# Performance work log

Hardware: AMD Instinct MI355X
Metric: run time of the kernel (lower is better)

The kernel has to match this reference:

```python
import jax, jax.numpy as jnp
import numpy as np

N_NODES = 50000
N_EDGES = 800000
N_GRAPHS = 128
HEADS = 4
HDIM = 32
N_CLASSES = 10
LEAKY_ALPHA = 0.2


def setup_inputs() -> dict:
    key = jax.random.key(0)
    ks = jax.random.split(key, 12)
    src = jax.random.randint(ks[0], (N_EDGES,), 0, N_NODES, dtype=jnp.int32)
    # guarantee every node has in-degree >= 1 so 3/deg is finite
    dst_tail = jax.random.randint(ks[1], (N_EDGES - N_NODES,), 0, N_NODES, dtype=jnp.int32)
    dst = jnp.concatenate([jnp.arange(N_NODES, dtype=jnp.int32), dst_tail])
    graph_ids = jnp.sort(jax.random.randint(ks[2], (N_NODES,), 0, N_GRAPHS, dtype=jnp.int32))
    s = 0.1
    return {
        "src": src,
        "dst": dst,
        "graph_ids": graph_ids,
        "W1": jax.random.normal(ks[3], (4, HEADS * HDIM), jnp.float32) * s,
        "al1": jax.random.normal(ks[4], (HEADS, HDIM), jnp.float32) * s,
        "ar1": jax.random.normal(ks[5], (HEADS, HDIM), jnp.float32) * s,
        "W2": jax.random.normal(ks[6], (HEADS * HDIM, HEADS * HDIM), jnp.float32) * s,
        "al2": jax.random.normal(ks[7], (HEADS, HDIM), jnp.float32) * s,
        "ar2": jax.random.normal(ks[8], (HEADS, HDIM), jnp.float32) * s,
        "Wc": jax.random.normal(ks[9], (HEADS * HDIM, N_CLASSES), jnp.float32) * s,
        "bc": jax.random.normal(ks[10], (N_CLASSES,), jnp.float32) * s,
    }


def _gat_layer(x, src, dst, W, al, ar):
    # x: [N, Fin]; W: [Fin, H*D]; al, ar: [H, D]
    n = x.shape[0]
    ft = (x @ W).reshape(n, HEADS, HDIM)                       # [N, H, D]
    a1 = jnp.einsum("nhd,hd->nh", ft, al)                      # [N, H]
    a2 = jnp.einsum("nhd,hd->nh", ft, ar)                      # [N, H]
    e = jax.nn.leaky_relu(a1[src] + a2[dst], LEAKY_ALPHA)      # [E, H]
    # segment softmax over incoming edges of each dst node
    m = jax.ops.segment_max(e, dst, num_segments=n)            # [N, H]
    m = jax.lax.stop_gradient(m)
    ex = jnp.exp(e - m[dst])                                   # [E, H]
    denom = jax.ops.segment_sum(ex, dst, num_segments=n)       # [N, H]
    alpha = ex / denom[dst]                                    # [E, H]
    # gather-multiply-scatter aggregation
    out = jax.ops.segment_sum(ft[src] * alpha[:, :, None], dst, num_segments=n)  # [N, H, D]
    return jax.nn.relu(out.reshape(n, HEADS * HDIM))


def reference(src, dst, graph_ids, W1, al1, ar1, W2, al2, ar2, Wc, bc):
    n = N_NODES
    ones_e = jnp.ones(src.shape[0], jnp.float32)
    deg = jax.ops.segment_sum(ones_e, dst, num_segments=n)     # in-degrees [N]
    h = jnp.stack(
        [deg, (deg - 3.0 > 0).astype(jnp.float32), 3.0 / deg, (deg - 4.0 > 0).astype(jnp.float32)],
        axis=1,
    )                                                          # [N, 4]
    h = _gat_layer(h, src, dst, W1, al1, ar1)                  # [N, H*D]
    h = _gat_layer(h, src, dst, W2, al2, ar2)                  # [N, H*D]
    # mean_nodes: per-graph mean pooling
    gsum = jax.ops.segment_sum(h, graph_ids, num_segments=N_GRAPHS)
    cnt = jax.ops.segment_sum(jnp.ones(n, jnp.float32), graph_ids, num_segments=N_GRAPHS)
    gmean = gsum / jnp.maximum(cnt, 1.0)[:, None]              # [G, H*D]
    return jax.nn.sigmoid(gmean @ Wc + bc)                     # [G, n_classes]
```

## Files before the change

### kernel.cpp

```cpp
#include <hip/hip_runtime.h>
#include <hip/hip_fp16.h>
#include <math.h>

#define HEADS 4
#define HDIM 32
#define FDIM 128
#define NGRAPH 128
#define NCLASS 10

#define NBW 128
#define NBP 512
#define BCAP 4096
#define SLICE 4096

typedef _Float16 h4_t __attribute__((ext_vector_type(4)));
typedef float f4_t __attribute__((ext_vector_type(4)));
typedef float f2_t __attribute__((ext_vector_type(2)));

__device__ __forceinline__ float lrelu(float x) { return fmaxf(x, 0.2f * x); }

__global__ void k_wfrag(const float* __restrict__ W2, __half* __restrict__ Wfrag,
                        float* __restrict__ gsum, int* __restrict__ gcnt,
                        int* __restrict__ bcur) {
    int gid = blockIdx.x * 256 + threadIdx.x;
    ((float4*)gsum)[gid] = make_float4(0.f, 0.f, 0.f, 0.f);
    if (gid < NGRAPH) gcnt[gid] = 0;
    if (gid < NBP) bcur[gid] = 0;
    int fid = gid >> 6, l = gid & 63;
    int ks = fid >> 3, t = fid & 7;
    int k0 = ks * 16 + 4 * (l >> 4);
    int n0 = t * 16 + (l & 15);
    __half2 lo = __floats2half2_rn(W2[(k0 + 0) * FDIM + n0], W2[(k0 + 1) * FDIM + n0]);
    __half2 hi = __floats2half2_rn(W2[(k0 + 2) * FDIM + n0], W2[(k0 + 3) * FDIM + n0]);
    size_t base = ((size_t)fid * 64 + l) * 4;
    *(__half2*)(Wfrag + base)     = lo;
    *(__half2*)(Wfrag + base + 2) = hi;
}

__global__ __launch_bounds__(256) void k_part(const int* __restrict__ src,
        const int* __restrict__ dst, int E, int* __restrict__ bcur,
        unsigned int* __restrict__ part) {
    __shared__ int lcnt[NBP];
    __shared__ int loff[NBP];
    __shared__ int lpos[NBP];
    __shared__ unsigned int staged[SLICE];
    __shared__ int tgt[SLICE];
    __shared__ int ws[4];
    int tid = threadIdx.x, lane = tid & 63, w = tid >> 6;
    int beg = blockIdx.x * SLICE, end = min(E, beg + SLICE);
    int m = end - beg;
    for (int i = tid; i < NBP; i += 256) lcnt[i] = 0;
    __syncthreads();
    for (int i = beg + tid; i < end; i += 256)
        atomicAdd(&lcnt[dst[i] >> 7], 1);
    __syncthreads();
    int c0 = lcnt[2 * tid], c1 = lcnt[2 * tid + 1];
    int t = c0 + c1;
    int incl = t;
    #pragma unroll
    for (int off = 1; off < 64; off <<= 1) {
        int y = __shfl_up(incl, off);
        if (lane >= off) incl += y;
    }
    if (lane == 63) ws[w] = incl;
    __syncthreads();
    int wpre = 0;
    #pragma unroll
    for (int j = 0; j < 4; ++j) if (j < w) wpre += ws[j];
    int ex = wpre + (incl - t);
    loff[2 * tid] = ex; loff[2 * tid + 1] = ex + c0;
    if (c0) lpos[2 * tid] = atomicAdd(&bcur[2 * tid], c0);
    if (c1) lpos[2 * tid + 1] = atomicAdd(&bcur[2 * tid + 1], c1);
    lcnt[2 * tid] = 0; lcnt[2 * tid + 1] = 0;
    __syncthreads();
    for (int i = beg + tid; i < end; i += 256) {
        int s = src[i], d = dst[i];
        int b = d >> 7;
        int idx = atomicAdd(&lcnt[b], 1);
        int slot = loff[b] + idx;
        staged[slot] = ((unsigned int)(d & (NBW - 1)) << 16) | (unsigned int)s;
        tgt[slot] = b * BCAP + lpos[b] + idx;
    }
    __syncthreads();
    for (int i = tid; i < m; i += 256)
        part[tgt[i]] = staged[i];
}

__global__ __launch_bounds__(256) void k_build(const unsigned int* __restrict__ part,
        const int* __restrict__ bcur, unsigned int* __restrict__ nodeinfo,
        unsigned short* __restrict__ csr, unsigned short* __restrict__ deg16, int n) {
    __shared__ int ldeg[NBW];
    __shared__ int loffs[NBW];
    __shared__ int wtot[2];
    int b = blockIdx.x, tid = threadIdx.x;
    int lane = tid & 63, w = tid >> 6;
    if (tid < NBW) ldeg[tid] = 0;
    __syncthreads();
    int beg = b * BCAP, end = beg + bcur[b];
    for (int i = beg + tid; i < end; i += 256)
        atomicAdd(&ldeg[part[i] >> 16], 1);
    __syncthreads();
    int x = (tid < NBW) ? ldeg[tid] : 0;
    int incl = x;
    #pragma unroll
    for (int off = 1; off < 64; off <<= 1) {
        int y = __shfl_up(incl, off);
        if (lane >= off) incl += y;
    }
    if (tid < NBW && lane == 63) wtot[w] = incl;
    __syncthreads();
    if (tid < NBW) {
        int pre = incl - x;
        if (w == 1) pre += wtot[0];
        loffs[tid] = beg + pre;
        int v = b * NBW + tid;
        if (v < n) {
            nodeinfo[v] = ((unsigned int)(beg + pre) << 9) | (unsigned int)x;
            deg16[v] = (unsigned short)x;
        }
    }
    __syncthreads();
    if (tid < NBW) ldeg[tid] = 0;
    __syncthreads();
    for (int i = beg + tid; i < end; i += 256) {
        unsigned int e = part[i];
        int lv = e >> 16;
        int p = atomicAdd(&ldeg[lv], 1);
        csr[loffs[lv] + p] = (unsigned short)(e & 0xffffu);
    }
}

__global__ __launch_bounds__(256) void k_agg1(const unsigned int* __restrict__ nodeinfo,
        const unsigned short* __restrict__ csr, const unsigned short* __restrict__ deg16,
        const float* __restrict__ W1, const float* __restrict__ al1,
        const float* __restrict__ ar1, float* __restrict__ Sbuf, int n) {
    __shared__ float wla[16], wlr[16];
    int tid = threadIdx.x;
    if (tid < 32) {
        int k = (tid & 15) >> 2, h = tid & 3;
        const float* av = (tid < 16) ? al1 : ar1;
        float s = 0.f;
        #pragma unroll
        for (int d = 0; d < 32; ++d) s += W1[k * FDIM + h * HDIM + d] * av[h * HDIM + d];
        if (tid < 16) wla[k * 4 + h] = s; else wlr[k * 4 + h] = s;
    }
    __syncthreads();
    int c = tid & 15;
    int v = blockIdx.x * 16 + (tid >> 4);
    if (v >= n) return;
    unsigned int info = nodeinfo[v];
    int beg = info >> 9;
    int dg = info & 511;
    float dv = (float)dg;
    float4 hvv = make_float4(dv, (dv - 3.0f > 0.0f) ? 1.0f : 0.0f, 3.0f / dv,
                             (dv - 4.0f > 0.0f) ? 1.0f : 0.0f);
    float a2h[4];
    #pragma unroll
    for (int h = 0; h < 4; ++h)
        a2h[h] = hvv.x * wlr[0 + h] + hvv.y * wlr[4 + h] + hvv.z * wlr[8 + h] + hvv.w * wlr[12 + h];
    float P[4][4], D[4];
    #pragma unroll
    for (int h = 0; h < 4; ++h) { D[h] = 0.f;
        #pragma unroll
        for (int d = 0; d < 4; ++d) P[h][d] = 0.f; }
    for (int j = beg + c; j < beg + dg; j += 16) {
        int u = csr[j];
        float du = (float)deg16[u];
        float4 fu = make_float4(du, (du - 3.0f > 0.0f) ? 1.0f : 0.0f, 3.0f / du,
                                (du - 4.0f > 0.0f) ? 1.0f : 0.0f);
        float wgt[4];
        #pragma unroll
        for (int h = 0; h < 4; ++h) {
            float a1h = fu.x * wla[0 + h] + fu.y * wla[4 + h] + fu.z * wla[8 + h] + fu.w * wla[12 + h];
            wgt[h] = __expf(lrelu(a1h + a2h[h]));
        }
        #pragma unroll
        for (int h = 0; h < 4; ++h) {
            D[h] += wgt[h];
            P[h][0] = fmaf(wgt[h], fu.x, P[h][0]);
            P[h][1] = fmaf(wgt[h], fu.y, P[h][1]);
            P[h][2] = fmaf(wgt[h], fu.z, P[h][2]);
            P[h][3] = fmaf(wgt[h], fu.w, P[h][3]);
        }
    }
    #pragma unroll
    for (int off = 1; off < 16; off <<= 1) {
        #pragma unroll
        for (int h = 0; h < 4; ++h) {
            D[h] += __shfl_xor(D[h], off);
            #pragma unroll
            for (int d = 0; d < 4; ++d) P[h][d] += __shfl_xor(P[h][d], off);
        }
    }
    if (c == 0) {
        #pragma unroll
        for (int h = 0; h < 4; ++h) {
            float r = 1.0f / D[h];
            *(float4*)(Sbuf + v * 16 + h * 4) =
                make_float4(P[h][0] * r, P[h][1] * r, P[h][2] * r, P[h][3] * r);
        }
    }
}

__global__ __launch_bounds__(256) void k_layer2(const float* __restrict__ Sbuf,
        const float* __restrict__ W1, const __half* __restrict__ Wfrag,
        const float* __restrict__ al, const float* __restrict__ ar,
        unsigned char* __restrict__ ft8, float* __restrict__ a1b,
        float* __restrict__ a2b, int n) {
    __shared__ __half Alds[4][16 * 132];
    int tid = threadIdx.x, l = tid & 63, w = tid >> 6;
    int c = l & 15, g = l >> 4;
    int v0 = (blockIdx.x * 4 + w) * 16;

    float2 w1c[4];
    #pragma unroll
    for (int d = 0; d < 4; ++d) w1c[d] = *(const float2*)(W1 + d * FDIM + 2 * l);
    for (int jj = 0; jj < 16; ++jj) {
        int v = min(v0 + jj, n - 1);
        float4 s = *(const float4*)(Sbuf + (size_t)v * 16 + g * 4);
        float t0 = s.x * w1c[0].x + s.y * w1c[1].x + s.z * w1c[2].x + s.w * w1c[3].x;
        float t1 = s.x * w1c[0].y + s.y * w1c[1].y + s.z * w1c[2].y + s.w * w1c[3].y;
        *(__half2*)(&Alds[w][jj * 132 + 2 * l]) = __floats2half2_rn(fmaxf(t0, 0.f), fmaxf(t1, 0.f));
    }
    __syncthreads();

    f4_t acc[8];
    #pragma unroll
    for (int t = 0; t < 8; ++t) acc[t] = (f4_t){0.f, 0.f, 0.f, 0.f};
    #pragma unroll
    for (int ks = 0; ks < 8; ++ks) {
        h4_t af = *(const h4_t*)(&Alds[w][c * 132 + ks * 16 + 4 * g]);
        #pragma unroll
        for (int t = 0; t < 8; ++t) {
            h4_t bf = *(const h4_t*)(Wfrag + ((size_t)(ks * 8 + t) * 64 + l) * 4);
            acc[t] = __builtin_amdgcn_mfma_f32_16x16x16f16(af, bf, acc[t], 0, 0, 0);
        }
    }

    #pragma unroll
    for (int t = 0; t < 8; ++t) {
        #pragma unroll
        for (int r = 0; r < 4; ++r) {
            int v = v0 + 4 * g + r;
            if (v < n) {
                int pk = __builtin_amdgcn_cvt_pk_fp8_f32(acc[t][r], acc[t][r], 0, false);
                ft8[(size_t)v * FDIM + t * 16 + c] = (unsigned char)(pk & 0xff);
            }
        }
    }
    float al0[4], al1v[4], ar0[4], ar1v[4];
    #pragma unroll
    for (int h = 0; h < 4; ++h) {
        al0[h] = al[h * 32 + c]; al1v[h] = al[h * 32 + 16 + c];
        ar0[h] = ar[h * 32 + c]; ar1v[h] = ar[h * 32 + 16 + c];
    }
    #pragma unroll
    for (int r = 0; r < 4; ++r) {
        int v = v0 + 4 * g + r;
        #pragma unroll
        for (int h = 0; h < 4; ++h) {
            float p1 = acc[2 * h][r] * al0[h] + acc[2 * h + 1][r] * al1v[h];
            float p2 = acc[2 * h][r] * ar0[h] + acc[2 * h + 1][r] * ar1v[h];
            #pragma unroll
            for (int off = 1; off < 16; off <<= 1) {
                p1 += __shfl_xor(p1, off);
                p2 += __shfl_xor(p2, off);
            }
            if (c == h && v < n) {
                a1b[v * 4 + h] = p1;
                a2b[v * 4 + h] = p2;
            }
        }
    }
}

__global__ __launch_bounds__(256) void k_agg2(const unsigned int* __restrict__ nodeinfo,
        const unsigned short* __restrict__ csr, const unsigned char* __restrict__ ft8,
        const float* __restrict__ a1, const float* __restrict__ a2,
        __half* __restrict__ out, int n) {
    int tid = threadIdx.x, lane = tid & 63, w = tid >> 6;
    int qw = lane >> 4, ql = lane & 15;
    int v = blockIdx.x * 16 + w * 4 + qw;
    if (v >= n) return;
    unsigned int info = nodeinfo[v];
    int beg = info >> 9, end = beg + (info & 511);
    int h = ql >> 2;
    float a2h = a2[v * 4 + h];
    float acc[8];
    #pragma unroll
    for (int k = 0; k < 8; ++k) acc[k] = 0.f;
    float dsum = 0.f;
    const unsigned char* fbase = ft8 + (size_t)ql * 8;
    int j = beg;
    for (; j + 4 <= end; j += 4) {
        int s[4];
        #pragma unroll
        for (int k = 0; k < 4; ++k) s[k] = csr[j + k];
        float wv[4]; uint2 bv[4];
        #pragma unroll
        for (int k = 0; k < 4; ++k) {
            wv[k] = __expf(lrelu(a1[s[k] * 4 + h] + a2h));
            bv[k] = *(const uint2*)(fbase + (size_t)s[k] * FDIM);
        }
        #pragma unroll
        for (int k = 0; k < 4; ++k) {
            dsum += wv[k];
            f2_t g;
            g = __builtin_amdgcn_cvt_pk_f32_fp8(bv[k].x, false); acc[0] = fmaf(wv[k], g[0], acc[0]); acc[1] = fmaf(wv[k], g[1], acc[1]);
            g = __builtin_amdgcn_cvt_pk_f32_fp8(bv[k].x, true);  acc[2] = fmaf(wv[k], g[0], acc[2]); acc[3] = fmaf(wv[k], g[1], acc[3]);
            g = __builtin_amdgcn_cvt_pk_f32_fp8(bv[k].y, false); acc[4] = fmaf(wv[k], g[0], acc[4]); acc[5] = fmaf(wv[k], g[1], acc[5]);
            g = __builtin_amdgcn_cvt_pk_f32_fp8(bv[k].y, true);  acc[6] = fmaf(wv[k], g[0], acc[6]); acc[7] = fmaf(wv[k], g[1], acc[7]);
        }
    }
    for (; j < end; ++j) {
        int s0 = csr[j];
        float w0 = __expf(lrelu(a1[s0 * 4 + h] + a2h));
        uint2 b0 = *(const uint2*)(fbase + (size_t)s0 * FDIM);
        dsum += w0;
        f2_t g;
        g = __builtin_amdgcn_cvt_pk_f32_fp8(b0.x, false); acc[0] = fmaf(w0, g[0], acc[0]); acc[1] = fmaf(w0, g[1], acc[1]);
        g = __builtin_amdgcn_cvt_pk_f32_fp8(b0.x, true);  acc[2] = fmaf(w0, g[0], acc[2]); acc[3] = fmaf(w0, g[1], acc[3]);
        g = __builtin_amdgcn_cvt_pk_f32_fp8(b0.y, false); acc[4] = fmaf(w0, g[0], acc[4]); acc[5] = fmaf(w0, g[1], acc[5]);
        g = __builtin_amdgcn_cvt_pk_f32_fp8(b0.y, true);  acc[6] = fmaf(w0, g[0], acc[6]); acc[7] = fmaf(w0, g[1], acc[7]);
    }
    float r = 1.0f / dsum;
    __half2 o[4];
    #pragma unroll
    for (int k = 0; k < 4; ++k)
        o[k] = __floats2half2_rn(fmaxf(acc[2 * k] * r, 0.f), fmaxf(acc[2 * k + 1] * r, 0.f));
    *(float4*)(out + (size_t)v * FDIM + ql * 8) = *(float4*)o;
}

__global__ void k_pool(const __half* __restrict__ hbuf, const int* __restrict__ gid,
                       float* __restrict__ gsum, int* __restrict__ gcnt, int n) {
    const int STRIP = 32;
    int wv = (blockIdx.x * blockDim.x + threadIdx.x) >> 6;
    int lane = threadIdx.x & 63;
    int beg = wv * STRIP;
    if (beg >= n) return;
    int end = min(beg + STRIP, n);
    int f = 2 * lane;
    float2 acc = make_float2(0.f, 0.f);
    int cur = gid[beg];
    int cnt = 0;
    for (int i = beg; i < end; ++i) {
        int g = gid[i];
        if (g != cur) {
            atomicAdd(&gsum[cur * FDIM + f], acc.x);
            atomicAdd(&gsum[cur * FDIM + f + 1], acc.y);
            if (lane == 0) atomicAdd(&gcnt[cur], cnt);
            acc = make_float2(0.f, 0.f); cnt = 0; cur = g;
        }
        float2 x = __half22float2(*(const __half2*)(hbuf + (size_t)i * FDIM + f));
        acc.x += x.x; acc.y += x.y; cnt++;
    }
    atomicAdd(&gsum[cur * FDIM + f], acc.x);
    atomicAdd(&gsum[cur * FDIM + f + 1], acc.y);
    if (lane == 0) atomicAdd(&gcnt[cur], cnt);
}

__global__ void k_classify(const float* __restrict__ gsum, const int* __restrict__ gcnt,
                           const float* __restrict__ Wc, const float* __restrict__ bc,
                           float* __restrict__ out) {
    int idx = blockIdx.x * blockDim.x + threadIdx.x;
    if (idx >= NGRAPH * NCLASS) return;
    int g = idx / NCLASS, c = idx % NCLASS;
    float rc = 1.0f / fmaxf((float)gcnt[g], 1.0f);
    float s = bc[c];
    for (int k = 0; k < FDIM; ++k)
        s += gsum[g * FDIM + k] * rc * Wc[k * NCLASS + c];
    out[idx] = 1.0f / (1.0f + __expf(-s));
}

extern "C" void kernel_launch(void* const* d_in, const int* in_sizes, int n_in,
                              void* d_out, int out_size, void* d_ws, size_t ws_size,
                              hipStream_t stream) {
    const int*   src = (const int*)d_in[0];
    const int*   dst = (const int*)d_in[1];
    const int*   gid = (const int*)d_in[2];
    const float* W1  = (const float*)d_in[3];
    const float* al1 = (const float*)d_in[4];
    const float* ar1 = (const float*)d_in[5];
    const float* W2  = (const float*)d_in[6];
    const float* al2 = (const float*)d_in[7];
    const float* ar2 = (const float*)d_in[8];
    const float* Wc  = (const float*)d_in[9];
    const float* bc  = (const float*)d_in[10];
    float* out = (float*)d_out;
    const int E = in_sizes[0];
    const int N = in_sizes[2];

    char* ws = (char*)d_ws;
    size_t off = 0;
    auto alloc = [&](size_t bytes) -> void* {
        void* p = ws + off;
        off = (off + bytes + 255) & ~(size_t)255;
        return p;
    };
    unsigned int*   part = (unsigned int*)alloc((size_t)NBP * BCAP * 4);
    unsigned short* csr  = (unsigned short*)alloc((size_t)NBP * BCAP * 2);
    int*    bcur   = (int*)alloc(NBP * 4);
    unsigned int* nodeinfo = (unsigned int*)alloc((size_t)N * 4);
    unsigned short* deg16  = (unsigned short*)alloc((size_t)N * 2);
    float*  Sbuf   = (float*)alloc((size_t)N * 16 * 4);
    float*  a1b    = (float*)alloc((size_t)N * HEADS * 4);
    float*  a2b    = (float*)alloc((size_t)N * HEADS * 4);
    unsigned char* ft8 = (unsigned char*)alloc((size_t)N * FDIM);
    __half* hbuf   = (__half*)alloc((size_t)N * FDIM * 2);
    __half* Wfrag  = (__half*)alloc((size_t)FDIM * FDIM * 2);
    float*  gsum   = (float*)alloc((size_t)NGRAPH * FDIM * 4);
    int*    gcnt   = (int*)alloc((size_t)NGRAPH * 4);

    int pb_edges = (E + SLICE - 1) / SLICE;
    int nb2 = (N + NBW - 1) / NBW;

    k_wfrag<<<16, 256, 0, stream>>>(W2, Wfrag, gsum, gcnt, bcur);
    k_part<<<pb_edges, 256, 0, stream>>>(src, dst, E, bcur, part);
    k_build<<<nb2, 256, 0, stream>>>(part, bcur, nodeinfo, csr, deg16, N);
    k_agg1<<<(N + 15) / 16, 256, 0, stream>>>(nodeinfo, csr, deg16, W1, al1, ar1, Sbuf, N);
    k_layer2<<<(N + 63) / 64, 256, 0, stream>>>(Sbuf, W1, Wfrag, al2, ar2, ft8, a1b, a2b, N);
    k_agg2<<<(N + 15) / 16, 256, 0, stream>>>(nodeinfo, csr, ft8, a1b, a2b, hbuf, N);

    int pb = (((N + 31) / 32) + 3) / 4;
    k_pool<<<pb, 256, 0, stream>>>(hbuf, gid, gsum, gcnt, N);
    k_classify<<<(NGRAPH * NCLASS + 255) / 256, 256, 0, stream>>>(gsum, gcnt, Wc, bc, out);
}
```

Before: 119.5 us.

## Split layer-2 GEMM output columns across wave pairs to double block count

```diff
diff --git a/kernel.cpp b/kernel.cpp
--- a/kernel.cpp
+++ b/kernel.cpp
@@ -207,68 +207,69 @@
         const float* __restrict__ al, const float* __restrict__ ar,
         unsigned char* __restrict__ ft8, float* __restrict__ a1b,
         float* __restrict__ a2b, int n) {
-    __shared__ __half Alds[4][16 * 132];
+    __shared__ __half Alds[2][16 * 132];
     int tid = threadIdx.x, l = tid & 63, w = tid >> 6;
+    int g2 = w >> 1, half = w & 1;
     int c = l & 15, g = l >> 4;
-    int v0 = (blockIdx.x * 4 + w) * 16;
+    int v0 = (blockIdx.x * 2 + g2) * 16;
 
     float2 w1c[4];
     #pragma unroll
     for (int d = 0; d < 4; ++d) w1c[d] = *(const float2*)(W1 + d * FDIM + 2 * l);
-    for (int jj = 0; jj < 16; ++jj) {
+    #pragma unroll
+    for (int jr = 0; jr < 8; ++jr) {
+        int jj = half * 8 + jr;
         int v = min(v0 + jj, n - 1);
         float4 s = *(const float4*)(Sbuf + (size_t)v * 16 + g * 4);
         float t0 = s.x * w1c[0].x + s.y * w1c[1].x + s.z * w1c[2].x + s.w * w1c[3].x;
         float t1 = s.x * w1c[0].y + s.y * w1c[1].y + s.z * w1c[2].y + s.w * w1c[3].y;
-        *(__half2*)(&Alds[w][jj * 132 + 2 * l]) = __floats2half2_rn(fmaxf(t0, 0.f), fmaxf(t1, 0.f));
-    }
-    __syncthreads();
-
-    f4_t acc[8];
-    #pragma unroll
-    for (int t = 0; t < 8; ++t) acc[t] = (f4_t){0.f, 0.f, 0.f, 0.f};
+        *(__half2*)(&Alds[g2][jj * 132 + 2 * l]) = __floats2half2_rn(fmaxf(t0, 0.f), fmaxf(t1, 0.f));
+    }
+    __syncthreads();
+
+    f4_t acc[4];
+    #pragma unroll
+    for (int t = 0; t < 4; ++t) acc[t] = (f4_t){0.f, 0.f, 0.f, 0.f};
     #pragma unroll
     for (int ks = 0; ks < 8; ++ks) {
-        h4_t af = *(const h4_t*)(&Alds[w][c * 132 + ks * 16 + 4 * g]);
-        #pragma unroll
-        for (int t = 0; t < 8; ++t) {
-            h4_t bf = *(const h4_t*)(Wfrag + ((size_t)(ks * 8 + t) * 64 + l) * 4);
+        h4_t af = *(const h4_t*)(&Alds[g2][c * 132 + ks * 16 + 4 * g]);
+        #pragma unroll
+        for (int t = 0; t < 4; ++t) {
+            h4_t bf = *(const h4_t*)(Wfrag + ((size_t)(ks * 8 + half * 4 + t) * 64 + l) * 4);
             acc[t] = __builtin_amdgcn_mfma_f32_16x16x16f16(af, bf, acc[t], 0, 0, 0);
         }
     }
 
     #pragma unroll
-    for (int t = 0; t < 8; ++t) {
+    for (int t = 0; t < 4; ++t) {
+        int tp = half * 4 + t;
         #pragma unroll
         for (int r = 0; r < 4; ++r) {
             int v = v0 + 4 * g + r;
             if (v < n) {
                 int pk = __builtin_amdgcn_cvt_pk_fp8_f32(acc[t][r], acc[t][r], 0, false);
-                ft8[(size_t)v * FDIM + t * 16 + c] = (unsigned char)(pk & 0xff);
+                ft8[(size_t)v * FDIM + tp * 16 + c] = (unsigned char)(pk & 0xff);
             }
         }
     }
-    float al0[4], al1v[4], ar0[4], ar1v[4];
-    #pragma unroll
-    for (int h = 0; h < 4; ++h) {
-        al0[h] = al[h * 32 + c]; al1v[h] = al[h * 32 + 16 + c];
-        ar0[h] = ar[h * 32 + c]; ar1v[h] = ar[h * 32 + 16 + c];
-    }
-    #pragma unroll
-    for (int r = 0; r < 4; ++r) {
-        int v = v0 + 4 * g + r;
-        #pragma unroll
-        for (int h = 0; h < 4; ++h) {
-            float p1 = acc[2 * h][r] * al0[h] + acc[2 * h + 1][r] * al1v[h];
-            float p2 = acc[2 * h][r] * ar0[h] + acc[2 * h + 1][r] * ar1v[h];
+    #pragma unroll
+    for (int hh = 0; hh < 2; ++hh) {
+        int hp = half * 2 + hh;
+        float al0 = al[hp * 32 + c], al1v = al[hp * 32 + 16 + c];
+        float ar0 = ar[hp * 32 + c], ar1v = ar[hp * 32 + 16 + c];
+        #pragma unroll
+        for (int r = 0; r < 4; ++r) {
+            int v = v0 + 4 * g + r;
+            float p1 = acc[2 * hh][r] * al0 + acc[2 * hh + 1][r] * al1v;
+            float p2 = acc[2 * hh][r] * ar0 + acc[2 * hh + 1][r] * ar1v;
             #pragma unroll
             for (int off = 1; off < 16; off <<= 1) {
                 p1 += __shfl_xor(p1, off);
                 p2 += __shfl_xor(p2, off);
             }
-            if (c == h && v < n) {
-                a1b[v * 4 + h] = p1;
-                a2b[v * 4 + h] = p2;
+            if (c == hp && v < n) {
+                a1b[v * 4 + hp] = p1;
+                a2b[v * 4 + hp] = p2;
             }
         }
     }
@@ -418,7 +419,7 @@
     k_part<<<pb_edges, 256, 0, stream>>>(src, dst, E, bcur, part);
     k_build<<<nb2, 256, 0, stream>>>(part, bcur, nodeinfo, csr, deg16, N);
     k_agg1<<<(N + 15) / 16, 256, 0, stream>>>(nodeinfo, csr, deg16, W1, al1, ar1, Sbuf, N);
-    k_layer2<<<(N + 63) / 64, 256, 0, stream>>>(Sbuf, W1, Wfrag, al2, ar2, ft8, a1b, a2b, N);
+    k_layer2<<<(N + 31) / 32, 256, 0, stream>>>(Sbuf, W1, Wfrag, al2, ar2, ft8, a1b, a2b, N);
     k_agg2<<<(N + 15) / 16, 256, 0, stream>>>(nodeinfo, csr, ft8, a1b, a2b, hbuf, N);
 
     int pb = (((N + 31) / 32) + 3) / 4;
```

Result: faster. 117.1 us, median of 2 (-2.0%).
